# Kernel optimization log

Hardware: AMD Instinct MI355X
Metric: run time of the kernel (lower is better)

The kernel has to match this reference:

```python
import jax, jax.numpy as jnp
import numpy as np

IN_DIM = 512
OUT_DIM = 256


def setup_inputs() -> dict:
    key = jax.random.key(0)
    ks = jax.random.split(key, 5)
    b, n, d, o = 32, 64, IN_DIM, OUT_DIM
    lim1 = 1.0 / np.sqrt(2 * d)
    lim2 = 1.0 / np.sqrt(o)
    return {
        "x": jax.random.normal(ks[0], (b, n, d), dtype=jnp.float32),
        "W1": jax.random.uniform(ks[1], (o, 2 * d), jnp.float32, -lim1, lim1),
        "b1": jax.random.uniform(ks[2], (o,), jnp.float32, -lim1, lim1),
        "W2": jax.random.uniform(ks[3], (o, o), jnp.float32, -lim2, lim2),
        "b2": jax.random.uniform(ks[4], (o,), jnp.float32, -lim2, lim2),
    }


def reference(x, W1, b1, W2, b2):
    # x: [b, n, d]; fc1 over cat(xi, xj) == xi @ Wa.T + xj @ Wb.T + b1
    b, n, d = x.shape
    Wa, Wb = W1[:, :d], W1[:, d:]
    hi = jnp.einsum("bnd,od->bno", x, Wa)  # [b, n, o]
    hj = jnp.einsum("bnd,od->bno", x, Wb)  # [b, n, o]
    h = hi[:, :, None, :] + hj[:, None, :, :] + b1  # [b, n, n, o]
    y = jax.nn.relu(jnp.einsum("bijo,po->bijp", h, W2) + b2)  # [b, n, n, o]
    mask = ~jnp.eye(n, dtype=bool)  # zero self-pairs
    y = y * mask[None, :, :, None]
    return y.sum(axis=2)  # [b, n, o]
```

## Files before the change

### kernel.cpp

```cpp
#include <hip/hip_runtime.h>
#include <hip/hip_bf16.h>


typedef unsigned short u16;
typedef __attribute__((ext_vector_type(8))) short short8v;
typedef __attribute__((ext_vector_type(4))) short short4v;
typedef __attribute__((ext_vector_type(4))) float float4v;
typedef __attribute__((ext_vector_type(2))) float float2v;

typedef __attribute__((address_space(1))) const unsigned char* gas_ptr;
typedef __attribute__((address_space(3))) unsigned char* las_ptr;

__device__ __forceinline__ void lds_load16(const void* g, void* l) {
    __builtin_amdgcn_global_load_lds((gas_ptr)g, (las_ptr)l, 16, 0, 0);
}

__device__ __forceinline__ u16 f2bf(float f) {
    unsigned u = __float_as_uint(f);
    return (u16)((u + 0x7fffu + ((u >> 16) & 1u)) >> 16);
}

__device__ __forceinline__ short8v cvt8v(float4v a, float4v b) {
    union { u16 us[8]; short8v v; } o;
    o.us[0] = f2bf(a.x); o.us[1] = f2bf(a.y); o.us[2] = f2bf(a.z); o.us[3] = f2bf(a.w);
    o.us[4] = f2bf(b.x); o.us[5] = f2bf(b.y); o.us[6] = f2bf(b.z); o.us[7] = f2bf(b.w);
    return o.v;
}

__global__ __launch_bounds__(256) void prep_kernel(
    const float* __restrict__ x, const float* __restrict__ W1,
    const float* __restrict__ b1, const float* __restrict__ W2,
    const float* __restrict__ b2,
    u16* __restrict__ Wfb, u16* __restrict__ xb, float* __restrict__ cvec) {
    const int bid = blockIdx.x;
    const int t = threadIdx.x;
    if (bid >= 65) {
        int base = (bid - 65) * 4096 + t * 16;
        const float* s = x + base;
        float4v a0 = *(const float4v*)s,        a1 = *(const float4v*)(s + 4);
        float4v a2 = *(const float4v*)(s + 8),  a3 = *(const float4v*)(s + 12);
        *(short8v*)&xb[base]     = cvt8v(a0, a1);
        *(short8v*)&xb[base + 8] = cvt8v(a2, a3);
        return;
    }
    if (bid == 64) {
        float acc = b2[t];
        const float4v* wrow = (const float4v*)(W2 + t * 256);
#pragma unroll 8
        for (int o4 = 0; o4 < 64; ++o4) {
            float4v wv = wrow[o4];
            float4v bv = *(const float4v*)(b1 + o4 * 4);
            acc += wv.x * bv.x + wv.y * bv.y + wv.z * bv.z + wv.w * bv.w;
        }
        cvec[t] = acc;
        return;
    }

    __shared__ __align__(16) u16 As[32 * 264];
    __shared__ __align__(16) u16 Bt[128 * 264];
    const int qt = bid >> 2, dt = bid & 3;
    const int q0 = qt * 32, d0 = dt * 128;
    const int pw = q0 & 255;
    const int off = (q0 & 256) * 2;
    const int lane = t & 63, w = t >> 6;
    const int rQ = lane >> 4, rM = lane & 15;

#pragma unroll
    for (int rr = 0; rr < 4; ++rr) {
        int row = w * 8 + rr * 2 + (lane >> 5);
        int c = lane & 31;
        const float* s = W2 + (pw + row) * 256 + c * 8;
        float4v a0 = *(const float4v*)s, a1 = *(const float4v*)(s + 4);
        *(short8v*)&As[row * 264 + c * 8] = cvt8v(a0, a1);
    }
#pragma unroll
    for (int s2 = 0; s2 < 2; ++s2) {
        const int u = t * 2 + s2;
        const int o0 = (u & 63) * 4;
        const int dbase = (u >> 6) * 16;
        const float* s0 = W1 + o0 * 1024 + off + d0 + dbase;
        float4v f[4][4];
#pragma unroll
        for (int j = 0; j < 4; ++j)
#pragma unroll
            for (int q4 = 0; q4 < 4; ++q4)
                f[j][q4] = *(const float4v*)(s0 + j * 1024 + q4 * 4);
        const int ubase = o0 >> 3, sub = o0 & 7;
#pragma unroll
        for (int dd = 0; dd < 16; ++dd) {
            int d = dbase + dd;
            int usw = ubase ^ ((d >> 3) & 7);
            union { u16 us[4]; short4v v; } pk;
            pk.us[0] = f2bf(f[0][dd >> 2][dd & 3]);
            pk.us[1] = f2bf(f[1][dd >> 2][dd & 3]);
            pk.us[2] = f2bf(f[2][dd >> 2][dd & 3]);
            pk.us[3] = f2bf(f[3][dd >> 2][dd & 3]);
            *(short4v*)&Bt[d * 264 + usw * 8 + sub] = pk.v;
        }
    }
    __syncthreads();

    const int qh = (w & 1) * 16, dq = (w >> 1) * 64;
    float4v acc[4] = {};
#pragma unroll
    for (int ks = 0; ks < 8; ++ks) {
        short8v a = *(const short8v*)&As[(qh + rM) * 264 + (ks * 4 + rQ) * 8];
#pragma unroll
        for (int nf = 0; nf < 4; ++nf) {
            int drow = dq + nf * 16 + rM;
            int ku = (ks * 4 + rQ) ^ ((drow >> 3) & 7);
            short8v bf = *(const short8v*)&Bt[drow * 264 + ku * 8];
            acc[nf] = __builtin_amdgcn_mfma_f32_16x16x32_bf16(a, bf, acc[nf], 0, 0, 0);
        }
    }
#pragma unroll
    for (int nf = 0; nf < 4; ++nf)
#pragma unroll
        for (int r = 0; r < 4; ++r) {
            int q = q0 + qh + rQ * 4 + r;
            int d = d0 + dq + nf * 16 + rM;
            Wfb[q * 512 + d] = f2bf(acc[nf][r]);
        }
}

#define UV_OFF 133120
#define FUSED_LDS (133120 + 2 * 64 * 34 * 4)

__global__ __launch_bounds__(512, 1) void fused_kernel(
    const u16* __restrict__ xb, const u16* __restrict__ Wfb,
    const float* __restrict__ cvec, float* __restrict__ out) {
    __shared__ __align__(16) unsigned char smem[FUSED_LDS];
    u16* Xs = (u16*)smem;
    u16* Ws = (u16*)smem + 64 * 520;
    float* Us = (float*)(smem + UV_OFF);
    float* Vs = Us + 64 * 34;
    const int bid = blockIdx.x;
    const int b = bid & 31, pc = bid >> 5;
    const int p0 = pc * 32;
    const int tid = threadIdx.x;
    const int lane = tid & 63, w = tid >> 6;
    const int rQ = lane >> 4, rM = lane & 15;
    const int uv = w & 1, rh = w >> 1;

#pragma unroll
    for (int rr = 0; rr < 8; ++rr) {
        int row = w * 8 + rr;
        int q = (row < 32) ? (p0 + row) : (256 + p0 + (row - 32));
        lds_load16(Wfb + q * 512 + lane * 8, (void*)&Ws[row * 520]);
    }
#pragma unroll
    for (int rr = 0; rr < 8; ++rr) {
        int row = w * 8 + rr;
        lds_load16(xb + (b * 64 + row) * 512 + lane * 8, (void*)&Xs[row * 520]);
    }
    __syncthreads();

    float4v acc[2] = {};
#pragma unroll
    for (int ks = 0; ks < 16; ++ks) {
        short8v a = *(const short8v*)&Xs[(rh * 16 + rM) * 520 + (ks * 4 + rQ) * 8];
#pragma unroll
        for (int nf = 0; nf < 2; ++nf) {
            int brow = uv * 32 + nf * 16 + rM;
            short8v bf = *(const short8v*)&Ws[brow * 520 + (ks * 4 + rQ) * 8];
            acc[nf] = __builtin_amdgcn_mfma_f32_16x16x32_bf16(a, bf, acc[nf], 0, 0, 0);
        }
    }

    float* dst = uv ? Vs : Us;
#pragma unroll
    for (int nf = 0; nf < 2; ++nf)
#pragma unroll
        for (int r = 0; r < 4; ++r)
            dst[(rh * 16 + rQ * 4 + r) * 34 + nf * 16 + rM] = acc[nf][r];
    __syncthreads();

    const int p2 = tid & 15;
    const int ig = tid >> 4;
    float2v cv = *(const float2v*)(cvec + p0 + p2 * 2);
    float2v u2[2], acc2[2];
#pragma unroll
    for (int ii = 0; ii < 2; ++ii) {
        float2v uu = *(const float2v*)&Us[(ig * 2 + ii) * 34 + p2 * 2];
        u2[ii].x = uu.x + cv.x; u2[ii].y = uu.y + cv.y;
        acc2[ii].x = 0.f; acc2[ii].y = 0.f;
    }
#pragma unroll 8
    for (int j = 0; j < 64; ++j) {
        float2v v = *(const float2v*)&Vs[j * 34 + p2 * 2];
#pragma unroll
        for (int ii = 0; ii < 2; ++ii) {
            acc2[ii].x += fmaxf(u2[ii].x + v.x, 0.f);
            acc2[ii].y += fmaxf(u2[ii].y + v.y, 0.f);
        }
    }
#pragma unroll
    for (int ii = 0; ii < 2; ++ii) {
        int i = ig * 2 + ii;
        float2v vd = *(const float2v*)&Vs[i * 34 + p2 * 2];
        acc2[ii].x -= fmaxf(u2[ii].x + vd.x, 0.f);
        acc2[ii].y -= fmaxf(u2[ii].y + vd.y, 0.f);
        *(float2v*)&out[(b * 64 + i) * 256 + p0 + p2 * 2] = acc2[ii];
    }
}

extern "C" void kernel_launch(void* const* d_in, const int* in_sizes, int n_in,
                              void* d_out, int out_size, void* d_ws, size_t ws_size,
                              hipStream_t stream) {
    const float* x  = (const float*)d_in[0];
    const float* W1 = (const float*)d_in[1];
    const float* b1 = (const float*)d_in[2];
    const float* W2 = (const float*)d_in[3];
    const float* b2 = (const float*)d_in[4];
    float* out = (float*)d_out;

    u16* Wfb = (u16*)d_ws;
    u16* xb  = Wfb + 512 * 512;
    float* cvec = (float*)(xb + 2048 * 512);

    prep_kernel<<<321, 256, 0, stream>>>(x, W1, b1, W2, b2, Wfb, xb, cvec);
    fused_kernel<<<256, 512, 0, stream>>>(xb, Wfb, cvec, out);
}
```

Measured before the change: 21.23 us.

## Halve per-block output tile, keep weight fragments in registers, double grid

Each fused block now covers 16 output columns instead of 32, and the launch grows to 512 blocks. The W fragments are loaded straight from global memory into registers instead of being staged through LDS, which cuts LDS use and lets more blocks fit on a CU (launch bounds raised to 4 blocks). Batch indices are also remapped across blocks. The trade-off is that each block reloads the 64x512 x tile, so the x tile is fetched twice as often overall, and register pressure rises from the 16 held fragments.

```diff
diff --git a/kernel.cpp b/kernel.cpp
--- a/kernel.cpp
+++ b/kernel.cpp
@@ -123,31 +123,29 @@
         }
 }
 
-#define UV_OFF 133120
-#define FUSED_LDS (133120 + 2 * 64 * 34 * 4)
-
-__global__ __launch_bounds__(512, 1) void fused_kernel(
+#define UVS 18
+__global__ __launch_bounds__(512, 4) void fused_kernel(
     const u16* __restrict__ xb, const u16* __restrict__ Wfb,
     const float* __restrict__ cvec, float* __restrict__ out) {
-    __shared__ __align__(16) unsigned char smem[FUSED_LDS];
-    u16* Xs = (u16*)smem;
-    u16* Ws = (u16*)smem + 64 * 520;
-    float* Us = (float*)(smem + UV_OFF);
-    float* Vs = Us + 64 * 34;
+    __shared__ __align__(16) u16 Xs[64 * 520];
+    __shared__ __align__(16) float UVs[2 * 64 * UVS];
+    float* Us = UVs;
+    float* Vs = UVs + 64 * UVS;
     const int bid = blockIdx.x;
-    const int b = bid & 31, pc = bid >> 5;
-    const int p0 = pc * 32;
+    const int b = ((bid & 7) << 2) | ((bid >> 3) & 3);
+    const int pc = bid >> 5;
+    const int p0 = pc * 16;
     const int tid = threadIdx.x;
     const int lane = tid & 63, w = tid >> 6;
     const int rQ = lane >> 4, rM = lane & 15;
     const int uv = w & 1, rh = w >> 1;
 
-#pragma unroll
-    for (int rr = 0; rr < 8; ++rr) {
-        int row = w * 8 + rr;
-        int q = (row < 32) ? (p0 + row) : (256 + p0 + (row - 32));
-        lds_load16(Wfb + q * 512 + lane * 8, (void*)&Ws[row * 520]);
-    }
+    const u16* wrow = Wfb + (uv * 256 + p0 + rM) * 512 + rQ * 8;
+    short8v bfrag[16];
+#pragma unroll
+    for (int ks = 0; ks < 16; ++ks)
+        bfrag[ks] = *(const short8v*)(wrow + ks * 32);
+
 #pragma unroll
     for (int rr = 0; rr < 8; ++rr) {
         int row = w * 8 + rr;
@@ -155,53 +153,36 @@
     }
     __syncthreads();
 
-    float4v acc[2] = {};
+    float4v acc = {};
 #pragma unroll
     for (int ks = 0; ks < 16; ++ks) {
         short8v a = *(const short8v*)&Xs[(rh * 16 + rM) * 520 + (ks * 4 + rQ) * 8];
-#pragma unroll
-        for (int nf = 0; nf < 2; ++nf) {
-            int brow = uv * 32 + nf * 16 + rM;
-            short8v bf = *(const short8v*)&Ws[brow * 520 + (ks * 4 + rQ) * 8];
-            acc[nf] = __builtin_amdgcn_mfma_f32_16x16x32_bf16(a, bf, acc[nf], 0, 0, 0);
-        }
+        acc = __builtin_amdgcn_mfma_f32_16x16x32_bf16(a, bfrag[ks], acc, 0, 0, 0);
     }
 
     float* dst = uv ? Vs : Us;
 #pragma unroll
-    for (int nf = 0; nf < 2; ++nf)
-#pragma unroll
-        for (int r = 0; r < 4; ++r)
-            dst[(rh * 16 + rQ * 4 + r) * 34 + nf * 16 + rM] = acc[nf][r];
+    for (int r = 0; r < 4; ++r)
+        dst[(rh * 16 + rQ * 4 + r) * UVS + rM] = acc[r];
     __syncthreads();
 
-    const int p2 = tid & 15;
-    const int ig = tid >> 4;
+    const int p2 = tid & 7;
+    const int i = tid >> 3;
     float2v cv = *(const float2v*)(cvec + p0 + p2 * 2);
-    float2v u2[2], acc2[2];
-#pragma unroll
-    for (int ii = 0; ii < 2; ++ii) {
-        float2v uu = *(const float2v*)&Us[(ig * 2 + ii) * 34 + p2 * 2];
-        u2[ii].x = uu.x + cv.x; u2[ii].y = uu.y + cv.y;
-        acc2[ii].x = 0.f; acc2[ii].y = 0.f;
-    }
+    float2v uu = *(const float2v*)&Us[i * UVS + p2 * 2];
+    float ux = uu.x + cv.x, uy = uu.y + cv.y;
+    float ax = 0.f, ay = 0.f;
 #pragma unroll 8
     for (int j = 0; j < 64; ++j) {
-        float2v v = *(const float2v*)&Vs[j * 34 + p2 * 2];
-#pragma unroll
-        for (int ii = 0; ii < 2; ++ii) {
-            acc2[ii].x += fmaxf(u2[ii].x + v.x, 0.f);
-            acc2[ii].y += fmaxf(u2[ii].y + v.y, 0.f);
-        }
-    }
-#pragma unroll
-    for (int ii = 0; ii < 2; ++ii) {
-        int i = ig * 2 + ii;
-        float2v vd = *(const float2v*)&Vs[i * 34 + p2 * 2];
-        acc2[ii].x -= fmaxf(u2[ii].x + vd.x, 0.f);
-        acc2[ii].y -= fmaxf(u2[ii].y + vd.y, 0.f);
-        *(float2v*)&out[(b * 64 + i) * 256 + p0 + p2 * 2] = acc2[ii];
-    }
+        float2v v = *(const float2v*)&Vs[j * UVS + p2 * 2];
+        ax += fmaxf(ux + v.x, 0.f);
+        ay += fmaxf(uy + v.y, 0.f);
+    }
+    float2v vd = *(const float2v*)&Vs[i * UVS + p2 * 2];
+    ax -= fmaxf(ux + vd.x, 0.f);
+    ay -= fmaxf(uy + vd.y, 0.f);
+    float2v res; res.x = ax; res.y = ay;
+    *(float2v*)&out[(b * 64 + i) * 256 + p0 + p2 * 2] = res;
 }
 
 extern "C" void kernel_launch(void* const* d_in, const int* in_sizes, int n_in,
@@ -219,5 +200,5 @@
     float* cvec = (float*)(xb + 2048 * 512);
 
     prep_kernel<<<321, 256, 0, stream>>>(x, W1, b1, W2, b2, Wfb, xb, cvec);
-    fused_kernel<<<256, 512, 0, stream>>>(xb, Wfb, cvec, out);
-}
+    fused_kernel<<<512, 512, 0, stream>>>(xb, Wfb, cvec, out);
+}
```

New measurement: 25.49 us. 1.2x slower.
